# Optimization experiments

Measured on AMD Instinct MI355X. Metric: run time of the kernel, lower is better.

The kernel has to match this reference:

```python
import jax, jax.numpy as jnp
import numpy as np

HEADS = 8
DIM = 512
SCALE = (DIM // HEADS) ** (-0.5)  # 0.125


def setup_inputs() -> dict:
    key = jax.random.key(0)
    k1, k2, k3, k4 = jax.random.split(key, 4)
    B, C, H, W = 4, DIM, 96, 96
    x = jax.random.normal(k1, (B, C, H, W), dtype=jnp.float32)
    # 1x1 conv weights collapsed to matrices [out_ch, in_ch]
    w_qkv = jax.random.normal(k2, (3 * DIM, DIM), dtype=jnp.float32) * (DIM ** -0.5)
    w_out = jax.random.normal(k3, (DIM, DIM), dtype=jnp.float32) * (DIM ** -0.5)
    b_out = jax.random.normal(k4, (DIM,), dtype=jnp.float32) * 0.01
    return {"x": x, "w_qkv": w_qkv, "w_out": w_out, "b_out": b_out}


def reference(x, w_qkv, w_out, b_out):
    # axis='height' branch of the original forward
    b, c, h, w = x.shape
    heads = HEADS
    d = c // heads
    # 1x1 conv == per-pixel GEMM: [B,3C,H,W]
    qkv = jnp.einsum('bchw,oc->bohw', x, w_qkv)
    # 'b (qkv heads d) x y -> qkv b heads x y d'
    qkv = qkv.reshape(b, 3, heads, d, h, w)
    qkv = jnp.transpose(qkv, (1, 0, 2, 4, 5, 3))  # [3, b, heads, h, w, d]
    q, k, v = qkv[0], qkv[1], qkv[2]
    # attention along the width axis, batched over (b, heads, row x)
    dots = jnp.einsum('bhxid,bhxjd->bhxij', q, k) * SCALE
    attn = jax.nn.softmax(dots, axis=-1)
    out = jnp.einsum('bhxij,bhxjd->bhxid', attn, v)  # [b, heads, h, w, d]
    # 'b heads x y d -> b (heads d) x y'
    out = jnp.transpose(out, (0, 1, 4, 2, 3)).reshape(b, heads * d, h, w)
    # to_out 1x1 conv with bias
    out = jnp.einsum('bchw,oc->bohw', out, w_out) + b_out[None, :, None, None]
    return out
```

## Files before the change

kernel.cpp:

```cpp
#include <hip/hip_runtime.h>

typedef unsigned short u16;
typedef unsigned int u32;
typedef __attribute__((ext_vector_type(8))) short short8;
typedef __attribute__((ext_vector_type(4))) float floatx4;

#define HEADS 8
#define DIM 512
#define HH 96
#define WW 96
#define NPIX 9216
#define M_TOT 36864
#define N_QKV 1536
#define SCALE 0.125f

__device__ __forceinline__ float b2f(u16 v){
    union{float f;u32 u;}x; x.u=((u32)v)<<16; return x.f;
}
__device__ __forceinline__ u16 f2b(float f){
    union{float f;u32 u;}x; x.f=f;
    u32 u=x.u + 0x7fffu + ((x.u>>16)&1u);
    return (u16)(u>>16);
}
__device__ __forceinline__ u32 pack2(float a,float b){
    return (u32)f2b(a) | ((u32)f2b(b)<<16);
}

__device__ __forceinline__ void gload16(const u16* g, u16* l){
    __builtin_amdgcn_global_load_lds(
        (const __attribute__((address_space(1))) u32*)g,
        (__attribute__((address_space(3))) u32*)l, 16, 0, 0);
}

__global__ void detect_dtype(const u16* __restrict__ wq, int* __restrict__ flag){
    __shared__ int cnt;
    if (threadIdx.x==0) cnt=0;
    __syncthreads();
    u16 u = wq[2*threadIdx.x];
    int e = (u>>7)&0xff;
    if (e>=100 && e<=128) atomicAdd(&cnt,1);
    __syncthreads();
    if (threadIdx.x==0) *flag = (cnt>128)?1:0;
}

__global__ __launch_bounds__(256)
void convert_w(const void* __restrict__ wq, const void* __restrict__ wo,
               const int* __restrict__ flag, u16* __restrict__ wqb, u16* __restrict__ wob){
    const int isb = *flag;
    int i = blockIdx.x*256 + threadIdx.x;
    const int nq = N_QKV*DIM;
    if (i < nq){
        wqb[i] = isb ? ((const u16*)wq)[i] : f2b(((const float*)wq)[i]);
    } else {
        int j = i - nq;
        wob[j] = isb ? ((const u16*)wo)[j] : f2b(((const float*)wo)[j]);
    }
}

__global__ __launch_bounds__(256)
void convert_x(const void* __restrict__ xv, const int* __restrict__ flag,
               u16* __restrict__ xb){
    __shared__ u16 tile[64][65];
    const int isb = *flag;
    const int p0 = blockIdx.x*64, c0 = blockIdx.y*64, b = blockIdx.z;
    const int t = threadIdx.x;
    const int pl = t&63, c4 = t>>6;
    const float* x32 = (const float*)xv;
    const u16*   x16 = (const u16*)xv;
    size_t src = ((size_t)b*DIM + c0 + c4)*NPIX + p0 + pl;
    #pragma unroll
    for (int i=0;i<16;i++){
        int cl = c4 + i*4;
        size_t s = src + (size_t)i*4*NPIX;
        tile[cl][pl] = isb ? x16[s] : f2b(x32[s]);
    }
    __syncthreads();
    const int cu = t&31, r8 = t>>5;
    u32* xb32 = (u32*)xb;
    #pragma unroll
    for (int i=0;i<8;i++){
        int pr = r8 + i*8;
        u32 v = (u32)tile[2*cu][pr] | ((u32)tile[2*cu+1][pr]<<16);
        xb32[((size_t)b*NPIX + p0 + pr)*(DIM/2) + (c0>>1) + cu] = v;
    }
}

__global__ __launch_bounds__(256)
void gemm_qkv(const u16* __restrict__ A, const u16* __restrict__ B,
              u16* __restrict__ Cqk, u16* __restrict__ vt){
    __shared__ __align__(16) union ShMem {
        struct { u16 A[8192]; u16 B[8192]; } s;
        float ct[4][16][68];
    } sh;
    const int id = blockIdx.x;
    const int xcd = id & 7, slot = id >> 3;
    const int by = xcd*36 + slot/12;
    const int bx = slot - (slot/12)*12;
    const int t = threadIdx.x;
    const int w = t>>6, l = t&63, lr = l&15, lq = l>>4;
    const int wm = w&1, wn = w>>1;
    const int n0 = bx*128;
    const int m0 = by*128;
    const u16* ag[4]; const u16* bg[4]; u16* al[4]; u16* bl[4];
    #pragma unroll
    for (int i=0;i<4;i++){
        int tt = w*4+i;
        int ks = tt>>3, sub = tt&7;
        ag[i] = A + (size_t)(m0 + sub*16 + lr)*DIM + ks*32 + lq*8;
        bg[i] = B + (size_t)(n0 + sub*16 + lr)*DIM + ks*32 + lq*8;
        al[i] = &sh.s.A[tt*512];
        bl[i] = &sh.s.B[tt*512];
    }
    floatx4 acc[4][4] = {};
    for (int kt=0; kt<DIM; kt+=64){
        #pragma unroll
        for (int i=0;i<4;i++){ gload16(ag[i]+kt, al[i]); gload16(bg[i]+kt, bl[i]); }
        __syncthreads();
        #pragma unroll
        for (int ks=0;ks<2;ks++){
            short8 a[4], b[4];
            #pragma unroll
            for (int mi=0;mi<4;mi++) a[mi] = *(const short8*)&sh.s.A[(ks*8 + wm*4 + mi)*512 + l*8];
            #pragma unroll
            for (int ni=0;ni<4;ni++) b[ni] = *(const short8*)&sh.s.B[(ks*8 + wn*4 + ni)*512 + l*8];
            #pragma unroll
            for (int mi=0;mi<4;mi++)
                #pragma unroll
                for (int ni=0;ni<4;ni++)
                    acc[mi][ni] = __builtin_amdgcn_mfma_f32_16x16x32_bf16(a[mi], b[ni], acc[mi][ni], 0,0,0);
        }
        __syncthreads();
    }
    if (bx < 8){
        #pragma unroll
        for (int mi=0;mi<4;mi++){
            #pragma unroll
            for (int ni=0;ni<4;ni++)
                #pragma unroll
                for (int r=0;r<4;r++)
                    sh.ct[w][lq*4+r][ni*16+lr] = acc[mi][ni][r];
            int row = l>>2, cg = l&3;
            const float* cp = &sh.ct[w][row][cg*16];
            float4 v0 = *(const float4*)(cp);
            float4 v1 = *(const float4*)(cp+4);
            float4 v2 = *(const float4*)(cp+8);
            float4 v3 = *(const float4*)(cp+12);
            uint4 s0, s1;
            s0.x=pack2(v0.x,v0.y); s0.y=pack2(v0.z,v0.w);
            s0.z=pack2(v1.x,v1.y); s0.w=pack2(v1.z,v1.w);
            s1.x=pack2(v2.x,v2.y); s1.y=pack2(v2.z,v2.w);
            s1.z=pack2(v3.x,v3.y); s1.w=pack2(v3.z,v3.w);
            u16* dst = Cqk + (size_t)(m0+wm*64+mi*16+row)*1024 + n0 + wn*64 + cg*16;
            *((uint4*)dst)     = s0;
            *((uint4*)(dst+8)) = s1;
        }
    } else {
        const int bat  = m0 / NPIX;
        const int pixb = m0 - bat*NPIX + wm*64;
        for (int ni=0; ni<4; ni++){
            #pragma unroll
            for (int mi=0;mi<4;mi++)
                #pragma unroll
                for (int r=0;r<4;r++)
                    sh.ct[w][lr][mi*16 + lq*4 + r] = acc[mi][ni][r];
            #pragma unroll
            for (int p=0;p<2;p++){
                int nl = (l>>3) + p*8;
                int ch = n0 + wn*64 + ni*16 + nl - 1024;
                int bh2 = bat*8 + (ch>>6);
                int dd  = ch & 63;
                const float* cp = &sh.ct[w][nl][(l&7)*8];
                float4 v0 = *(const float4*)cp;
                float4 v1 = *(const float4*)(cp+4);
                uint4 s;
                s.x=pack2(v0.x,v0.y); s.y=pack2(v0.z,v0.w);
                s.z=pack2(v1.x,v1.y); s.w=pack2(v1.z,v1.w);
                *(uint4*)(vt + (size_t)(bh2*64+dd)*NPIX + pixb + (l&7)*8) = s;
            }
        }
    }
}

__global__ __launch_bounds__(256)
void attn_kernel(const u16* __restrict__ qk, const u16* __restrict__ vt,
                 u16* __restrict__ attno){
    __shared__ __align__(16) u16 Qf[6144];
    __shared__ __align__(16) u16 Pb[9984];
    __shared__ float Ss[96][97];
    __shared__ float smax[96][2], ssum[96][2], rinv[96];
    const int t = threadIdx.x;
    const int w = t>>6, l = t&63, lr = l&15, lq = l>>4;
    const int wm = w&1, wn = w>>1;
    const int blk = blockIdx.x;
    const int row  = blk % HH;
    const int bh   = blk / HH;
    const int head = bh & 7;
    const int bat  = bh >> 3;
    const size_t pixrow = (size_t)bat*NPIX + row*WW;
    const u16* qbase = qk + pixrow*1024 + head*64;
    #pragma unroll
    for (int i=0;i<6;i++){
        int c  = w*6 + i;
        int c2 = (c<12) ? c : (c-12);
        int mt = c2>>1, ks = c2&1;
        const u16* g = qbase + (size_t)(mt*16+lr)*1024 + ks*32 + lq*8 + ((c<12)?0:512);
        u16* dst = ((c<12)?Qf:Pb) + c2*512 + l*8;
        gload16(g, dst);
    }
    __syncthreads();
    {
        floatx4 acc[3][3] = {};
        #pragma unroll
        for (int ks=0;ks<2;ks++){
            short8 af[3], bf[3];
            #pragma unroll
            for (int i=0;i<3;i++) af[i] = *(const short8*)&Qf[((wm*3+i)*2+ks)*512 + l*8];
            #pragma unroll
            for (int j=0;j<3;j++) bf[j] = *(const short8*)&Pb[((wn*3+j)*2+ks)*512 + l*8];
            #pragma unroll
            for (int i=0;i<3;i++)
                #pragma unroll
                for (int j=0;j<3;j++)
                    acc[i][j] = __builtin_amdgcn_mfma_f32_16x16x32_bf16(af[i], bf[j], acc[i][j], 0,0,0);
        }
        #pragma unroll
        for (int i=0;i<3;i++)
            #pragma unroll
            for (int j=0;j<3;j++)
                #pragma unroll
                for (int r=0;r<4;r++)
                    Ss[(wm*3+i)*16 + lq*4 + r][(wn*3+j)*16 + lr] = acc[i][j][r]*SCALE;
    }
    __syncthreads();
    #pragma unroll
    for (int i=0;i<3;i++){
        const u16* g = vt + (size_t)(bh*64 + w*16 + lr)*NPIX + row*WW + i*32 + lq*8;
        gload16(g, Qf + (w*3+i)*512 + l*8);
    }
    const int srow = t>>1, shalf = t&1, sbase = shalf*48;
    if (t < 192){
        float m = -1e30f;
        #pragma unroll 8
        for (int j=0;j<48;j++) m = fmaxf(m, Ss[srow][sbase+j]);
        smax[srow][shalf] = m;
    }
    __syncthreads();
    if (t < 192){
        float m2 = fmaxf(smax[srow][0], smax[srow][1]);
        float s = 0.f;
        u32* prow = (u32*)&Pb[srow*104 + sbase];
        #pragma unroll 8
        for (int j=0;j<48;j+=2){
            float e0 = __expf(Ss[srow][sbase+j]   - m2);
            float e1 = __expf(Ss[srow][sbase+j+1] - m2);
            prow[j>>1] = pack2(e0, e1);
            s += e0 + e1;
        }
        ssum[srow][shalf] = s;
    }
    __syncthreads();
    if (t < 192 && shalf==0) rinv[srow] = 1.f/(ssum[srow][0]+ssum[srow][1]);
    floatx4 o[3][2] = {};
    #pragma unroll
    for (int ks2=0;ks2<3;ks2++){
        short8 bf2[2];
        #pragma unroll
        for (int bb=0;bb<2;bb++)
            bf2[bb] = *(const short8*)&Qf[((wn*2+bb)*3+ks2)*512 + l*8];
        #pragma unroll
        for (int aa=0;aa<3;aa++){
            short8 af = *(const short8*)&Pb[((wm*3+aa)*16+lr)*104 + ks2*32 + lq*8];
            #pragma unroll
            for (int bb=0;bb<2;bb++)
                o[aa][bb] = __builtin_amdgcn_mfma_f32_16x16x32_bf16(af, bf2[bb], o[aa][bb], 0,0,0);
        }
    }
    __syncthreads();
    #pragma unroll
    for (int aa=0;aa<3;aa++){
        #pragma unroll
        for (int r=0;r<4;r++){
            int m = (wm*3+aa)*16 + lq*4 + r;
            float rv = rinv[m];
            int d0 = wn*32 + lr;
            Pb[m*72 + d0]      = f2b(o[aa][0][r]*rv);
            Pb[m*72 + d0 + 16] = f2b(o[aa][1][r]*rv);
        }
    }
    __syncthreads();
    #pragma unroll
    for (int i=0;i<3;i++){
        int idx = i*256 + t;
        int rr = idx>>3, seg = idx&7;
        uint4 vv = *(const uint4*)&Pb[rr*72 + seg*8];
        *(uint4*)(attno + (pixrow+rr)*512 + head*64 + seg*8) = vv;
    }
}

__global__ __launch_bounds__(256)
void gemm_out(const u16* __restrict__ A, const u16* __restrict__ B,
              const void* __restrict__ bias, const int* __restrict__ flag,
              void* __restrict__ outv){
    __shared__ __align__(16) union ShMem {
        struct { u16 A[8192]; u16 B[8192]; } s;
        float ct[4][16][68];
    } sh;
    const int id = blockIdx.x;
    const int xcd = id & 7, slot = id >> 3;
    const int by = xcd*36 + (slot>>2);
    const int bx = slot & 3;
    const int t = threadIdx.x;
    const int w = t>>6, l = t&63, lr = l&15, lq = l>>4;
    const int wm = w&1, wn = w>>1;
    const int n0 = bx*128;
    const int m0 = by*128;
    const u16* ag[4]; const u16* bg[4]; u16* al[4]; u16* bl[4];
    #pragma unroll
    for (int i=0;i<4;i++){
        int tt = w*4+i;
        int ks = tt>>3, sub = tt&7;
        ag[i] = A + (size_t)(m0 + sub*16 + lr)*DIM + ks*32 + lq*8;
        bg[i] = B + (size_t)(n0 + sub*16 + lr)*DIM + ks*32 + lq*8;
        al[i] = &sh.s.A[tt*512];
        bl[i] = &sh.s.B[tt*512];
    }
    floatx4 acc[4][4] = {};
    for (int kt=0; kt<DIM; kt+=64){
        #pragma unroll
        for (int i=0;i<4;i++){ gload16(ag[i]+kt, al[i]); gload16(bg[i]+kt, bl[i]); }
        __syncthreads();
        #pragma unroll
        for (int ks=0;ks<2;ks++){
            short8 a[4], b[4];
            #pragma unroll
            for (int mi=0;mi<4;mi++) a[mi] = *(const short8*)&sh.s.A[(ks*8 + wm*4 + mi)*512 + l*8];
            #pragma unroll
            for (int ni=0;ni<4;ni++) b[ni] = *(const short8*)&sh.s.B[(ks*8 + wn*4 + ni)*512 + l*8];
            #pragma unroll
            for (int mi=0;mi<4;mi++)
                #pragma unroll
                for (int ni=0;ni<4;ni++)
                    acc[mi][ni] = __builtin_amdgcn_mfma_f32_16x16x32_bf16(a[mi], b[ni], acc[mi][ni], 0,0,0);
        }
        __syncthreads();
    }
    const int isb = *flag;
    const int bat  = m0 / NPIX;
    const int pix0 = m0 - bat*NPIX + wm*64;
    const u16*   b16 = (const u16*)bias;
    const float* b32 = (const float*)bias;
    for (int ni=0; ni<4; ni++){
        #pragma unroll
        for (int mi=0;mi<4;mi++)
            #pragma unroll
            for (int r=0;r<4;r++)
                sh.ct[w][lr][mi*16 + lq*4 + r] = acc[mi][ni][r];
        #pragma unroll
        for (int p=0;p<2;p++){
            int nl = (l>>3) + p*8;
            int ng = n0 + wn*64 + ni*16 + nl;
            float bv = isb ? b2f(b16[ng]) : b32[ng];
            const float* cp = &sh.ct[w][nl][(l&7)*8];
            float4 v0 = *(const float4*)cp;
            float4 v1 = *(const float4*)(cp+4);
            v0.x+=bv; v0.y+=bv; v0.z+=bv; v0.w+=bv;
            v1.x+=bv; v1.y+=bv; v1.z+=bv; v1.w+=bv;
            size_t off = ((size_t)(bat*DIM + ng))*NPIX + pix0 + (l&7)*8;
            if (isb){
                uint4 s;
                s.x=pack2(v0.x,v0.y); s.y=pack2(v0.z,v0.w);
                s.z=pack2(v1.x,v1.y); s.w=pack2(v1.z,v1.w);
                *(uint4*)((u16*)outv + off) = s;
            } else {
                float* of = (float*)outv + off;
                *(float4*)of     = v0;
                *(float4*)(of+4) = v1;
            }
        }
    }
}

extern "C" void kernel_launch(void* const* d_in, const int* in_sizes, int n_in,
                              void* d_out, int out_size, void* d_ws, size_t ws_size,
                              hipStream_t stream){
    const void* x    = d_in[0];
    const void* wqkv = d_in[1];
    const void* wout = d_in[2];
    const void* bout = d_in[3];
    char* wsb = (char*)d_ws;
    int* flag    = (int*)wsb;
    u16* xb      = (u16*)(wsb + 256);
    u16* attn_ws = xb;
    u16* wqb     = xb + (size_t)M_TOT*DIM;
    u16* wob     = wqb + (size_t)N_QKV*DIM;
    u16* qk_ws   = wob + (size_t)DIM*DIM;
    u16* vt_ws   = qk_ws + (size_t)M_TOT*1024;
    detect_dtype<<<1, 256, 0, stream>>>((const u16*)wqkv, flag);
    convert_w<<<4096, 256, 0, stream>>>(wqkv, wout, flag, wqb, wob);
    convert_x<<<dim3(144, 8, 4), 256, 0, stream>>>(x, flag, xb);
    gemm_qkv<<<3456, 256, 0, stream>>>(xb, wqb, qk_ws, vt_ws);
    attn_kernel<<<3072, 256, 0, stream>>>(qk_ws, vt_ws, attn_ws);
    gemm_out<<<1152, 256, 0, stream>>>(attn_ws, wob, bout, flag, d_out);
}
```

Before: 372.4 us.

## Rewrite QKV and output GEMMs as 256x256 double-buffered 8-wave tiles

Both projection GEMMs move from 128x128 tiles with 4 waves and a single LDS buffer to 256x256 tiles with 8 waves and two 64 KB LDS stages. The next K-tile's global-to-LDS loads are interleaved between MFMA groups under raised wave priority. The aim is to hide global load latency behind matrix math and raise data reuse per LDS load. Epilogues are widened to write 32- or 16-element runs per lane. The cost is higher register pressure (32 accumulators per wave) and fewer, larger blocks (864 and 288), which may leave parts of the device idle for the smaller output GEMM.

New measurement: 347.2 us. -6.8%, faster.

```diff
diff --git a/kernel.cpp b/kernel.cpp
--- a/kernel.cpp
+++ b/kernel.cpp
@@ -85,62 +85,138 @@
     }
 }
 
-__global__ __launch_bounds__(256)
+__global__ __launch_bounds__(512, 2)
 void gemm_qkv(const u16* __restrict__ A, const u16* __restrict__ B,
               u16* __restrict__ Cqk, u16* __restrict__ vt){
     __shared__ __align__(16) union ShMem {
-        struct { u16 A[8192]; u16 B[8192]; } s;
-        float ct[4][16][68];
+        u16 tiles[65536];
+        float ctQ[8][16][68];
+        float ctV[8][16][132];
     } sh;
+    u16* lds = sh.tiles;
     const int id = blockIdx.x;
     const int xcd = id & 7, slot = id >> 3;
-    const int by = xcd*36 + slot/12;
-    const int bx = slot - (slot/12)*12;
+    const int q6 = slot/6;
+    const int by = xcd*18 + q6;
+    const int bx = slot - q6*6;
     const int t = threadIdx.x;
     const int w = t>>6, l = t&63, lr = l&15, lq = l>>4;
-    const int wm = w&1, wn = w>>1;
-    const int n0 = bx*128;
-    const int m0 = by*128;
-    const u16* ag[4]; const u16* bg[4]; u16* al[4]; u16* bl[4];
-    #pragma unroll
-    for (int i=0;i<4;i++){
-        int tt = w*4+i;
-        int ks = tt>>3, sub = tt&7;
-        ag[i] = A + (size_t)(m0 + sub*16 + lr)*DIM + ks*32 + lq*8;
-        bg[i] = B + (size_t)(n0 + sub*16 + lr)*DIM + ks*32 + lq*8;
-        al[i] = &sh.s.A[tt*512];
-        bl[i] = &sh.s.B[tt*512];
-    }
-    floatx4 acc[4][4] = {};
-    for (int kt=0; kt<DIM; kt+=64){
-        #pragma unroll
-        for (int i=0;i<4;i++){ gload16(ag[i]+kt, al[i]); gload16(bg[i]+kt, bl[i]); }
-        __syncthreads();
-        #pragma unroll
-        for (int ks=0;ks<2;ks++){
-            short8 a[4], b[4];
-            #pragma unroll
-            for (int mi=0;mi<4;mi++) a[mi] = *(const short8*)&sh.s.A[(ks*8 + wm*4 + mi)*512 + l*8];
-            #pragma unroll
-            for (int ni=0;ni<4;ni++) b[ni] = *(const short8*)&sh.s.B[(ks*8 + wn*4 + ni)*512 + l*8];
-            #pragma unroll
-            for (int mi=0;mi<4;mi++)
-                #pragma unroll
-                for (int ni=0;ni<4;ni++)
-                    acc[mi][ni] = __builtin_amdgcn_mfma_f32_16x16x32_bf16(a[mi], b[ni], acc[mi][ni], 0,0,0);
-        }
-        __syncthreads();
-    }
-    if (bx < 8){
+    const int wm2 = w>>2, wn4 = w&3;
+    const int m0 = by*256, n0 = bx*256;
+    const u16* gA0 = A + (size_t)(m0 +       w*16 + lr)*DIM + lq*8;
+    const u16* gA1 = A + (size_t)(m0 + 128 + w*16 + lr)*DIM + lq*8;
+    const u16* gB0 = B + (size_t)(n0 +       w*16 + lr)*DIM + lq*8;
+    const u16* gB1 = B + (size_t)(n0 + 128 + w*16 + lr)*DIM + lq*8;
+
+#define STG(gp, opb, h, ko, bb) do { \
+        const u16* _g = (gp) + (ko); \
+        u16* _l = lds + (bb)*32768 + (opb) + ((h)*8 + w)*1024; \
+        gload16(_g,      _l); \
+        gload16(_g + 32, _l + 512); \
+    } while(0)
+
+    floatx4 acc[8][4] = {};
+    STG(gA0, 0,     0, 0, 0);
+    STG(gA1, 0,     1, 0, 0);
+    STG(gB0, 16384, 0, 0, 0);
+    STG(gB1, 16384, 1, 0, 0);
+
+    #pragma unroll 1
+    for (int ktile=0; ktile<8; ++ktile){
+        const int cur = ktile&1, nxt = cur^1;
+        const int ko = (ktile+1)*64;
+        if (ktile < 7){
+            STG(gA0, 0, 0, ko, nxt);
+            asm volatile("s_waitcnt vmcnt(2)" ::: "memory");
+        } else {
+            asm volatile("s_waitcnt vmcnt(0)" ::: "memory");
+        }
+        __builtin_amdgcn_s_barrier();
+        asm volatile("" ::: "memory");
+        const u16* bA = lds + cur*32768 +         wm2*8192 + l*8;
+        const u16* bB = lds + cur*32768 + 16384 + wn4*4096 + l*8;
+        short8 af[4][2], bf[2][2];
         #pragma unroll
         for (int mi=0;mi<4;mi++){
+            af[mi][0] = *(const short8*)(bA + mi*1024);
+            af[mi][1] = *(const short8*)(bA + mi*1024 + 512);
+        }
+        #pragma unroll
+        for (int ni=0;ni<2;ni++){
+            bf[ni][0] = *(const short8*)(bB + ni*1024);
+            bf[ni][1] = *(const short8*)(bB + ni*1024 + 512);
+        }
+        if (ktile < 7) STG(gA1, 0, 1, ko, nxt);
+        __builtin_amdgcn_s_setprio(1);
+        #pragma unroll
+        for (int mi=0;mi<4;mi++)
+            #pragma unroll
+            for (int ni=0;ni<2;ni++){
+                acc[mi][ni] = __builtin_amdgcn_mfma_f32_16x16x32_bf16(af[mi][0], bf[ni][0], acc[mi][ni], 0,0,0);
+                acc[mi][ni] = __builtin_amdgcn_mfma_f32_16x16x32_bf16(af[mi][1], bf[ni][1], acc[mi][ni], 0,0,0);
+            }
+        __builtin_amdgcn_s_setprio(0);
+        #pragma unroll
+        for (int ni=0;ni<2;ni++){
+            bf[ni][0] = *(const short8*)(bB + (2+ni)*1024);
+            bf[ni][1] = *(const short8*)(bB + (2+ni)*1024 + 512);
+        }
+        if (ktile < 7) STG(gB0, 16384, 0, ko, nxt);
+        __builtin_amdgcn_s_setprio(1);
+        #pragma unroll
+        for (int mi=0;mi<4;mi++)
+            #pragma unroll
+            for (int ni=0;ni<2;ni++){
+                acc[mi][2+ni] = __builtin_amdgcn_mfma_f32_16x16x32_bf16(af[mi][0], bf[ni][0], acc[mi][2+ni], 0,0,0);
+                acc[mi][2+ni] = __builtin_amdgcn_mfma_f32_16x16x32_bf16(af[mi][1], bf[ni][1], acc[mi][2+ni], 0,0,0);
+            }
+        __builtin_amdgcn_s_setprio(0);
+        #pragma unroll
+        for (int mi=0;mi<4;mi++){
+            af[mi][0] = *(const short8*)(bA + (4+mi)*1024);
+            af[mi][1] = *(const short8*)(bA + (4+mi)*1024 + 512);
+        }
+        if (ktile < 7) STG(gB1, 16384, 1, ko, nxt);
+        __builtin_amdgcn_s_setprio(1);
+        #pragma unroll
+        for (int mi=0;mi<4;mi++)
+            #pragma unroll
+            for (int ni=0;ni<2;ni++){
+                acc[4+mi][2+ni] = __builtin_amdgcn_mfma_f32_16x16x32_bf16(af[mi][0], bf[ni][0], acc[4+mi][2+ni], 0,0,0);
+                acc[4+mi][2+ni] = __builtin_amdgcn_mfma_f32_16x16x32_bf16(af[mi][1], bf[ni][1], acc[4+mi][2+ni], 0,0,0);
+            }
+        __builtin_amdgcn_s_setprio(0);
+        #pragma unroll
+        for (int ni=0;ni<2;ni++){
+            bf[ni][0] = *(const short8*)(bB + ni*1024);
+            bf[ni][1] = *(const short8*)(bB + ni*1024 + 512);
+        }
+        __builtin_amdgcn_s_setprio(1);
+        #pragma unroll
+        for (int mi=0;mi<4;mi++)
+            #pragma unroll
+            for (int ni=0;ni<2;ni++){
+                acc[4+mi][ni] = __builtin_amdgcn_mfma_f32_16x16x32_bf16(af[mi][0], bf[ni][0], acc[4+mi][ni], 0,0,0);
+                acc[4+mi][ni] = __builtin_amdgcn_mfma_f32_16x16x32_bf16(af[mi][1], bf[ni][1], acc[4+mi][ni], 0,0,0);
+            }
+        __builtin_amdgcn_s_setprio(0);
+        asm volatile("" ::: "memory");
+        __builtin_amdgcn_s_barrier();
+        asm volatile("" ::: "memory");
+    }
+#undef STG
+    if (bx < 4){
+        float (*ct)[68] = sh.ctQ[w];
+        const int row = l>>2, cg = l&3;
+        u16* dstbase = Cqk + (size_t)(m0 + wm2*128)*1024 + n0 + wn4*64 + cg*16;
+        #pragma unroll
+        for (int mi=0;mi<8;mi++){
             #pragma unroll
             for (int ni=0;ni<4;ni++)
                 #pragma unroll
                 for (int r=0;r<4;r++)
-                    sh.ct[w][lq*4+r][ni*16+lr] = acc[mi][ni][r];
-            int row = l>>2, cg = l&3;
-            const float* cp = &sh.ct[w][row][cg*16];
+                    ct[lq*4+r][ni*16+lr] = acc[mi][ni][r];
+            const float* cp = &ct[row][cg*16];
             float4 v0 = *(const float4*)(cp);
             float4 v1 = *(const float4*)(cp+4);
             float4 v2 = *(const float4*)(cp+8);
@@ -150,33 +226,47 @@
             s0.z=pack2(v1.x,v1.y); s0.w=pack2(v1.z,v1.w);
             s1.x=pack2(v2.x,v2.y); s1.y=pack2(v2.z,v2.w);
             s1.z=pack2(v3.x,v3.y); s1.w=pack2(v3.z,v3.w);
-            u16* dst = Cqk + (size_t)(m0+wm*64+mi*16+row)*1024 + n0 + wn*64 + cg*16;
+            u16* dst = dstbase + (size_t)(mi*16 + row)*1024;
             *((uint4*)dst)     = s0;
             *((uint4*)(dst+8)) = s1;
         }
     } else {
+        float (*ct)[132] = sh.ctV[w];
         const int bat  = m0 / NPIX;
-        const int pixb = m0 - bat*NPIX + wm*64;
+        const int pixb = m0 - bat*NPIX + wm2*128;
+        const int nl = l>>2, seg = l&3;
         for (int ni=0; ni<4; ni++){
             #pragma unroll
-            for (int mi=0;mi<4;mi++)
+            for (int mi=0;mi<8;mi++)
                 #pragma unroll
                 for (int r=0;r<4;r++)
-                    sh.ct[w][lr][mi*16 + lq*4 + r] = acc[mi][ni][r];
-            #pragma unroll
-            for (int p=0;p<2;p++){
-                int nl = (l>>3) + p*8;
-                int ch = n0 + wn*64 + ni*16 + nl - 1024;
-                int bh2 = bat*8 + (ch>>6);
-                int dd  = ch & 63;
-                const float* cp = &sh.ct[w][nl][(l&7)*8];
-                float4 v0 = *(const float4*)cp;
-                float4 v1 = *(const float4*)(cp+4);
-                uint4 s;
-                s.x=pack2(v0.x,v0.y); s.y=pack2(v0.z,v0.w);
-                s.z=pack2(v1.x,v1.y); s.w=pack2(v1.z,v1.w);
-                *(uint4*)(vt + (size_t)(bh2*64+dd)*NPIX + pixb + (l&7)*8) = s;
-            }
+                    ct[lr][mi*16 + lq*4 + r] = acc[mi][ni][r];
+            int ch  = n0 + wn4*64 + ni*16 + nl - 1024;
+            int bh2 = bat*8 + (ch>>6);
+            int dd  = ch & 63;
+            const float* cp = &ct[nl][seg*32];
+            float4 v0 = *(const float4*)(cp);
+            float4 v1 = *(const float4*)(cp+4);
+            float4 v2 = *(const float4*)(cp+8);
+            float4 v3 = *(const float4*)(cp+12);
+            float4 v4 = *(const float4*)(cp+16);
+            float4 v5 = *(const float4*)(cp+20);
+            float4 v6 = *(const float4*)(cp+24);
+            float4 v7 = *(const float4*)(cp+28);
+            uint4 s0, s1, s2, s3;
+            s0.x=pack2(v0.x,v0.y); s0.y=pack2(v0.z,v0.w);
+            s0.z=pack2(v1.x,v1.y); s0.w=pack2(v1.z,v1.w);
+            s1.x=pack2(v2.x,v2.y); s1.y=pack2(v2.z,v2.w);
+            s1.z=pack2(v3.x,v3.y); s1.w=pack2(v3.z,v3.w);
+            s2.x=pack2(v4.x,v4.y); s2.y=pack2(v4.z,v4.w);
+            s2.z=pack2(v5.x,v5.y); s2.w=pack2(v5.z,v5.w);
+            s3.x=pack2(v6.x,v6.y); s3.y=pack2(v6.z,v6.w);
+            s3.z=pack2(v7.x,v7.y); s3.w=pack2(v7.z,v7.w);
+            u16* dst = vt + (size_t)(bh2*64+dd)*NPIX + pixb + seg*32;
+            *((uint4*)dst)      = s0;
+            *((uint4*)(dst+8))  = s1;
+            *((uint4*)(dst+16)) = s2;
+            *((uint4*)(dst+24)) = s3;
         }
     }
 }
@@ -297,84 +387,167 @@
     }
 }
 
-__global__ __launch_bounds__(256)
+__global__ __launch_bounds__(512, 2)
 void gemm_out(const u16* __restrict__ A, const u16* __restrict__ B,
               const void* __restrict__ bias, const int* __restrict__ flag,
               void* __restrict__ outv){
     __shared__ __align__(16) union ShMem {
-        struct { u16 A[8192]; u16 B[8192]; } s;
-        float ct[4][16][68];
+        u16 tiles[65536];
+        float ctV[8][16][132];
     } sh;
+    u16* lds = sh.tiles;
     const int id = blockIdx.x;
     const int xcd = id & 7, slot = id >> 3;
-    const int by = xcd*36 + (slot>>2);
-    const int bx = slot & 3;
+    const int by = xcd*18 + (slot>>1);
+    const int bx = slot & 1;
     const int t = threadIdx.x;
     const int w = t>>6, l = t&63, lr = l&15, lq = l>>4;
-    const int wm = w&1, wn = w>>1;
-    const int n0 = bx*128;
-    const int m0 = by*128;
-    const u16* ag[4]; const u16* bg[4]; u16* al[4]; u16* bl[4];
-    #pragma unroll
-    for (int i=0;i<4;i++){
-        int tt = w*4+i;
-        int ks = tt>>3, sub = tt&7;
-        ag[i] = A + (size_t)(m0 + sub*16 + lr)*DIM + ks*32 + lq*8;
-        bg[i] = B + (size_t)(n0 + sub*16 + lr)*DIM + ks*32 + lq*8;
-        al[i] = &sh.s.A[tt*512];
-        bl[i] = &sh.s.B[tt*512];
-    }
-    floatx4 acc[4][4] = {};
-    for (int kt=0; kt<DIM; kt+=64){
-        #pragma unroll
-        for (int i=0;i<4;i++){ gload16(ag[i]+kt, al[i]); gload16(bg[i]+kt, bl[i]); }
-        __syncthreads();
-        #pragma unroll
-        for (int ks=0;ks<2;ks++){
-            short8 a[4], b[4];
-            #pragma unroll
-            for (int mi=0;mi<4;mi++) a[mi] = *(const short8*)&sh.s.A[(ks*8 + wm*4 + mi)*512 + l*8];
-            #pragma unroll
-            for (int ni=0;ni<4;ni++) b[ni] = *(const short8*)&sh.s.B[(ks*8 + wn*4 + ni)*512 + l*8];
-            #pragma unroll
-            for (int mi=0;mi<4;mi++)
-                #pragma unroll
-                for (int ni=0;ni<4;ni++)
-                    acc[mi][ni] = __builtin_amdgcn_mfma_f32_16x16x32_bf16(a[mi], b[ni], acc[mi][ni], 0,0,0);
-        }
-        __syncthreads();
-    }
+    const int wm2 = w>>2, wn4 = w&3;
+    const int m0 = by*256, n0 = bx*256;
+    const u16* gA0 = A + (size_t)(m0 +       w*16 + lr)*DIM + lq*8;
+    const u16* gA1 = A + (size_t)(m0 + 128 + w*16 + lr)*DIM + lq*8;
+    const u16* gB0 = B + (size_t)(n0 +       w*16 + lr)*DIM + lq*8;
+    const u16* gB1 = B + (size_t)(n0 + 128 + w*16 + lr)*DIM + lq*8;
+
+#define STG(gp, opb, h, ko, bb) do { \
+        const u16* _g = (gp) + (ko); \
+        u16* _l = lds + (bb)*32768 + (opb) + ((h)*8 + w)*1024; \
+        gload16(_g,      _l); \
+        gload16(_g + 32, _l + 512); \
+    } while(0)
+
+    floatx4 acc[8][4] = {};
+    STG(gA0, 0,     0, 0, 0);
+    STG(gA1, 0,     1, 0, 0);
+    STG(gB0, 16384, 0, 0, 0);
+    STG(gB1, 16384, 1, 0, 0);
+
+    #pragma unroll 1
+    for (int ktile=0; ktile<8; ++ktile){
+        const int cur = ktile&1, nxt = cur^1;
+        const int ko = (ktile+1)*64;
+        if (ktile < 7){
+            STG(gA0, 0, 0, ko, nxt);
+            asm volatile("s_waitcnt vmcnt(2)" ::: "memory");
+        } else {
+            asm volatile("s_waitcnt vmcnt(0)" ::: "memory");
+        }
+        __builtin_amdgcn_s_barrier();
+        asm volatile("" ::: "memory");
+        const u16* bA = lds + cur*32768 +         wm2*8192 + l*8;
+        const u16* bB = lds + cur*32768 + 16384 + wn4*4096 + l*8;
+        short8 af[4][2], bf[2][2];
+        #pragma unroll
+        for (int mi=0;mi<4;mi++){
+            af[mi][0] = *(const short8*)(bA + mi*1024);
+            af[mi][1] = *(const short8*)(bA + mi*1024 + 512);
+        }
+        #pragma unroll
+        for (int ni=0;ni<2;ni++){
+            bf[ni][0] = *(const short8*)(bB + ni*1024);
+            bf[ni][1] = *(const short8*)(bB + ni*1024 + 512);
+        }
+        if (ktile < 7) STG(gA1, 0, 1, ko, nxt);
+        __builtin_amdgcn_s_setprio(1);
+        #pragma unroll
+        for (int mi=0;mi<4;mi++)
+            #pragma unroll
+            for (int ni=0;ni<2;ni++){
+                acc[mi][ni] = __builtin_amdgcn_mfma_f32_16x16x32_bf16(af[mi][0], bf[ni][0], acc[mi][ni], 0,0,0);
+                acc[mi][ni] = __builtin_amdgcn_mfma_f32_16x16x32_bf16(af[mi][1], bf[ni][1], acc[mi][ni], 0,0,0);
+            }
+        __builtin_amdgcn_s_setprio(0);
+        #pragma unroll
+        for (int ni=0;ni<2;ni++){
+            bf[ni][0] = *(const short8*)(bB + (2+ni)*1024);
+            bf[ni][1] = *(const short8*)(bB + (2+ni)*1024 + 512);
+        }
+        if (ktile < 7) STG(gB0, 16384, 0, ko, nxt);
+        __builtin_amdgcn_s_setprio(1);
+        #pragma unroll
+        for (int mi=0;mi<4;mi++)
+            #pragma unroll
+            for (int ni=0;ni<2;ni++){
+                acc[mi][2+ni] = __builtin_amdgcn_mfma_f32_16x16x32_bf16(af[mi][0], bf[ni][0], acc[mi][2+ni], 0,0,0);
+                acc[mi][2+ni] = __builtin_amdgcn_mfma_f32_16x16x32_bf16(af[mi][1], bf[ni][1], acc[mi][2+ni], 0,0,0);
+            }
+        __builtin_amdgcn_s_setprio(0);
+        #pragma unroll
+        for (int mi=0;mi<4;mi++){
+            af[mi][0] = *(const short8*)(bA + (4+mi)*1024);
+            af[mi][1] = *(const short8*)(bA + (4+mi)*1024 + 512);
+        }
+        if (ktile < 7) STG(gB1, 16384, 1, ko, nxt);
+        __builtin_amdgcn_s_setprio(1);
+        #pragma unroll
+        for (int mi=0;mi<4;mi++)
+            #pragma unroll
+            for (int ni=0;ni<2;ni++){
+                acc[4+mi][2+ni] = __builtin_amdgcn_mfma_f32_16x16x32_bf16(af[mi][0], bf[ni][0], acc[4+mi][2+ni], 0,0,0);
+                acc[4+mi][2+ni] = __builtin_amdgcn_mfma_f32_16x16x32_bf16(af[mi][1], bf[ni][1], acc[4+mi][2+ni], 0,0,0);
+            }
+        __builtin_amdgcn_s_setprio(0);
+        #pragma unroll
+        for (int ni=0;ni<2;ni++){
+            bf[ni][0] = *(const short8*)(bB + ni*1024);
+            bf[ni][1] = *(const short8*)(bB + ni*1024 + 512);
+        }
+        __builtin_amdgcn_s_setprio(1);
+        #pragma unroll
+        for (int mi=0;mi<4;mi++)
+            #pragma unroll
+            for (int ni=0;ni<2;ni++){
+                acc[4+mi][ni] = __builtin_amdgcn_mfma_f32_16x16x32_bf16(af[mi][0], bf[ni][0], acc[4+mi][ni], 0,0,0);
+                acc[4+mi][ni] = __builtin_amdgcn_mfma_f32_16x16x32_bf16(af[mi][1], bf[ni][1], acc[4+mi][ni], 0,0,0);
+            }
+        __builtin_amdgcn_s_setprio(0);
+        asm volatile("" ::: "memory");
+        __builtin_amdgcn_s_barrier();
+        asm volatile("" ::: "memory");
+    }
+#undef STG
     const int isb = *flag;
     const int bat  = m0 / NPIX;
-    const int pix0 = m0 - bat*NPIX + wm*64;
+    const int pix0 = m0 - bat*NPIX + wm2*128;
+    float (*ct)[132] = sh.ctV[w];
     const u16*   b16 = (const u16*)bias;
     const float* b32 = (const float*)bias;
+    const int nl = l>>3, seg8 = l&7;
     for (int ni=0; ni<4; ni++){
         #pragma unroll
-        for (int mi=0;mi<4;mi++)
+        for (int mi=0;mi<8;mi++)
             #pragma unroll
             for (int r=0;r<4;r++)
-                sh.ct[w][lr][mi*16 + lq*4 + r] = acc[mi][ni][r];
+                ct[lr][mi*16 + lq*4 + r] = acc[mi][ni][r];
         #pragma unroll
         for (int p=0;p<2;p++){
-            int nl = (l>>3) + p*8;
-            int ng = n0 + wn*64 + ni*16 + nl;
+            int nrow = nl + p*8;
+            int ng = n0 + wn4*64 + ni*16 + nrow;
             float bv = isb ? b2f(b16[ng]) : b32[ng];
-            const float* cp = &sh.ct[w][nl][(l&7)*8];
-            float4 v0 = *(const float4*)cp;
+            const float* cp = &ct[nrow][seg8*16];
+            float4 v0 = *(const float4*)(cp);
             float4 v1 = *(const float4*)(cp+4);
+            float4 v2 = *(const float4*)(cp+8);
+            float4 v3 = *(const float4*)(cp+12);
             v0.x+=bv; v0.y+=bv; v0.z+=bv; v0.w+=bv;
             v1.x+=bv; v1.y+=bv; v1.z+=bv; v1.w+=bv;
-            size_t off = ((size_t)(bat*DIM + ng))*NPIX + pix0 + (l&7)*8;
+            v2.x+=bv; v2.y+=bv; v2.z+=bv; v2.w+=bv;
+            v3.x+=bv; v3.y+=bv; v3.z+=bv; v3.w+=bv;
+            size_t off = ((size_t)(bat*DIM + ng))*NPIX + pix0 + seg8*16;
             if (isb){
-                uint4 s;
-                s.x=pack2(v0.x,v0.y); s.y=pack2(v0.z,v0.w);
-                s.z=pack2(v1.x,v1.y); s.w=pack2(v1.z,v1.w);
-                *(uint4*)((u16*)outv + off) = s;
+                uint4 s0, s1;
+                s0.x=pack2(v0.x,v0.y); s0.y=pack2(v0.z,v0.w);
+                s0.z=pack2(v1.x,v1.y); s0.w=pack2(v1.z,v1.w);
+                s1.x=pack2(v2.x,v2.y); s1.y=pack2(v2.z,v2.w);
+                s1.z=pack2(v3.x,v3.y); s1.w=pack2(v3.z,v3.w);
+                *(uint4*)((u16*)outv + off)     = s0;
+                *(uint4*)((u16*)outv + off + 8) = s1;
             } else {
                 float* of = (float*)outv + off;
-                *(float4*)of     = v0;
-                *(float4*)(of+4) = v1;
+                *(float4*)(of)    = v0;
+                *(float4*)(of+4)  = v1;
+                *(float4*)(of+8)  = v2;
+                *(float4*)(of+12) = v3;
             }
         }
     }
@@ -398,7 +571,7 @@
     detect_dtype<<<1, 256, 0, stream>>>((const u16*)wqkv, flag);
     convert_w<<<4096, 256, 0, stream>>>(wqkv, wout, flag, wqb, wob);
     convert_x<<<dim3(144, 8, 4), 256, 0, stream>>>(x, flag, xb);
-    gemm_qkv<<<3456, 256, 0, stream>>>(xb, wqb, qk_ws, vt_ws);
+    gemm_qkv<<<864, 512, 0, stream>>>(xb, wqb, qk_ws, vt_ws);
     attn_kernel<<<3072, 256, 0, stream>>>(qk_ws, vt_ws, attn_ws);
-    gemm_out<<<1152, 256, 0, stream>>>(attn_ws, wob, bout, flag, d_out);
-}
+    gemm_out<<<288, 512, 0, stream>>>(attn_ws, wob, bout, flag, d_out);
+}
```
